# Optimization experiments

Measured on AMD Instinct MI355X. Metric: run time of the kernel, lower is better.

## Reference

```python
import jax, jax.numpy as jnp
import numpy as np
from jax import lax

D_MODEL = 512
NUM_HEADS = 8
HEADDIM = D_MODEL // NUM_HEADS      # 64
EXPAND = 2
D_INNER = EXPAND * D_MODEL          # 1024
D_STATE = 64
NGROUPS = 1
KCONV = 4                           # window_size -> depthwise conv kernel
NHEADS = D_INNER // HEADDIM         # 16 SSM heads
D_FF = 2048
CONV_DIM = D_INNER + 2 * NGROUPS * D_STATE          # 1152 (x, B, C)
D_IN_PROJ = 2 * D_INNER + 2 * NGROUPS * D_STATE + NHEADS  # 2192 (z, x, B, C, dt)
EPS = 1e-6


def _rmsnorm(x, eps=EPS):
    return x * lax.rsqrt(jnp.mean(x * x, axis=-1, keepdims=True) + eps)


def _silu(x):
    return x * jax.nn.sigmoid(x)


def _ssm_scan(xs, dt, A, Bm, Cm):
    # xs: [B,L,H,P], dt: [B,L,H], A: [H], Bm/Cm: [B,L,N]  (ngroups=1 broadcast over heads)
    dA = jnp.exp(dt * A)                 # [B,L,H] decay per step
    dBx = dt[..., None] * xs             # [B,L,H,P] input contribution
    h0 = jnp.zeros((xs.shape[0], xs.shape[2], xs.shape[3], Bm.shape[2]), xs.dtype)

    def step(h, t):
        dA_t, dBx_t, B_t, C_t = t        # [B,H],[B,H,P],[B,N],[B,N]
        h = dA_t[..., None, None] * h + dBx_t[..., None] * B_t[:, None, None, :]
        y = jnp.einsum('bhpn,bn->bhp', h, C_t)
        return h, y

    _, ys = lax.scan(step, h0, (dA.transpose(1, 0, 2), dBx.transpose(1, 0, 2, 3),
                                Bm.transpose(1, 0, 2), Cm.transpose(1, 0, 2)))
    return ys.transpose(1, 0, 2, 3)      # [B,L,H,P]


def setup_inputs() -> dict:
    key = jax.random.key(0)
    ks = jax.random.split(key, 12)
    B, L = 8, 2048
    s = 0.02
    inp = {
        'x': jax.random.normal(ks[0], (B, L, D_MODEL), jnp.float32),
        'mask': jnp.ones((B, L), jnp.float32),
        'W_in': jax.random.normal(ks[1], (D_MODEL, D_IN_PROJ), jnp.float32) * s,
        'conv_w': jax.random.normal(ks[2], (CONV_DIM, KCONV), jnp.float32) * 0.1,
        'conv_b': jnp.zeros((CONV_DIM,), jnp.float32),
        'dt_bias': jax.random.normal(ks[3], (NHEADS,), jnp.float32) * 0.1,
        'A_log': jnp.log(jnp.arange(1, NHEADS + 1, dtype=jnp.float32)),
        'D': jnp.ones((NHEADS,), jnp.float32),
        'norm_w': jnp.ones((D_INNER,), jnp.float32),
        'W_out': jax.random.normal(ks[4], (D_INNER, D_MODEL), jnp.float32) * s,
        'W1': jax.random.normal(ks[5], (D_MODEL, D_FF), jnp.float32) * s,
        'b1': jnp.zeros((D_FF,), jnp.float32),
        'W2': jax.random.normal(ks[6], (D_FF, D_MODEL), jnp.float32) * s,
        'b2': jnp.zeros((D_MODEL,), jnp.float32),
    }
    return inp


def reference(x, mask, W_in, conv_w, conv_b, dt_bias, A_log, D, norm_w, W_out, W1, b1, W2, b2):
    B, L, _ = x.shape
    x = x * mask[..., None]
    u = _rmsnorm(x)

    zxbcdt = u @ W_in                                   # [B,L,2192]
    z = zxbcdt[..., :D_INNER]
    xBC = zxbcdt[..., D_INNER:D_INNER + CONV_DIM]
    dt = zxbcdt[..., D_INNER + CONV_DIM:]               # [B,L,H]

    # causal depthwise conv1d, kernel KCONV
    pad = jnp.pad(xBC, ((0, 0), (KCONV - 1, 0), (0, 0)))
    xBC = sum(pad[:, i:i + L, :] * conv_w[:, i] for i in range(KCONV)) + conv_b
    xBC = _silu(xBC) * mask[..., None]

    xs = xBC[..., :D_INNER].reshape(B, L, NHEADS, HEADDIM)
    Bm = xBC[..., D_INNER:D_INNER + D_STATE]            # [B,L,N] (ngroups=1)
    Cm = xBC[..., D_INNER + D_STATE:]

    dt = jax.nn.softplus(dt + dt_bias)
    A = -jnp.exp(A_log)                                 # [H]

    # bidirectional (non-causal) selective scan: forward + reversed scans
    y_f = _ssm_scan(xs, dt, A, Bm, Cm)
    y_b = _ssm_scan(xs[:, ::-1], dt[:, ::-1], A, Bm[:, ::-1], Cm[:, ::-1])[:, ::-1]
    y = y_f + y_b + D[None, None, :, None] * xs         # [B,L,H,P]
    y = y.reshape(B, L, D_INNER)

    # gated RMSNorm then output projection
    y = _rmsnorm(y * _silu(z)) * norm_w
    m = y @ W_out                                       # mamba2 output, [B,L,D]

    x = m + m                                           # x = x + dropout1(x) with x := mamba out
    h = _rmsnorm(x)
    x = x + (jax.nn.gelu(h @ W1 + b1) @ W2 + b2)        # x + mlp(norm2(x))
    return (x, m, dt, z)
```

## Files before the change

### kernel.cpp

```cpp
#include <hip/hip_runtime.h>
#include <cstdint>
#include <cstddef>

#define L_SEQ   2048
#define NROWS   16384
#define D_MODEL 512
#define D_INNER 1024
#define D_STATE 64
#define NHEADS  16
#define CONV_DIM 1152
#define D_IN_PROJ 2192
#define D_FF 2048
#define EPS 1e-6f

typedef __bf16 bf16_t;
typedef __bf16 bf16x8 __attribute__((ext_vector_type(8)));
typedef __bf16 bf16x4 __attribute__((ext_vector_type(4)));
typedef float  f32x4  __attribute__((ext_vector_type(4)));

#define OFF_WT_IN    0ull
#define OFF_WT_OUT   2244608ull
#define OFF_W1T      3293184ull
#define OFF_W2T      5390336ull
#define OFF_U        7487488ull
#define OFF_XBC_RAW  24264704ull
#define OFF_XBC_CONV 99762176ull
#define OFF_Y2       175259648ull
#define OFF_YN       242368512ull

__device__ __forceinline__ void gl_lds16(const void* g, void* s) {
  __builtin_amdgcn_global_load_lds(
      (__attribute__((address_space(1))) void*)(void*)g,
      (__attribute__((address_space(3))) void*)s, 16, 0, 0);
}

__device__ __forceinline__ float block_sum256(float v, float* red) {
#pragma unroll
  for (int o = 32; o > 0; o >>= 1) v += __shfl_xor(v, o, 64);
  int w = threadIdx.x >> 6;
  if ((threadIdx.x & 63) == 0) red[w] = v;
  __syncthreads();
  return red[0] + red[1] + red[2] + red[3];
}

__device__ __forceinline__ float softplus_f(float x) {
  return (x > 20.f) ? x : log1pf(expf(x));
}
__device__ __forceinline__ float silu_f(float x) {
  return x / (1.f + expf(-x));
}
__device__ __forceinline__ float gelu_tanh_f(float x) {
  float x3 = x * x * x;
  return 0.5f * x * (1.f + tanhf(0.7978845608f * (x + 0.044715f * x3)));
}

__global__ __launch_bounds__(256) void prep_weights_kernel(
    const float* __restrict__ W_in, const float* __restrict__ W_out,
    const float* __restrict__ W1, const float* __restrict__ W2,
    bf16_t* __restrict__ wt_in, bf16_t* __restrict__ wt_out,
    bf16_t* __restrict__ w1t, bf16_t* __restrict__ w2t) {
  const int S1 = D_IN_PROJ * 512;
  const int S2 = 512 * 1024;
  const int S3 = 2048 * 512;
  const int S4 = 512 * 2048;
  const int total = S1 + S2 + S3 + S4;
  for (int i = blockIdx.x * 256 + threadIdx.x; i < total; i += gridDim.x * 256) {
    if (i < S1) {
      int n = i / 512, k = i - n * 512;
      wt_in[i] = (bf16_t)W_in[k * D_IN_PROJ + n];
    } else if (i < S1 + S2) {
      int j = i - S1; int n = j >> 10, k = j & 1023;
      wt_out[j] = (bf16_t)W_out[k * 512 + n];
    } else if (i < S1 + S2 + S3) {
      int j = i - S1 - S2; int n = j >> 9, k = j & 511;
      w1t[j] = (bf16_t)W1[k * 2048 + n];
    } else {
      int j = i - S1 - S2 - S3; int n = j >> 11, k = j & 2047;
      w2t[j] = (bf16_t)W2[k * 512 + n];
    }
  }
}

__global__ __launch_bounds__(256) void rmsnorm_in_kernel(
    const float* __restrict__ x, const float* __restrict__ mask,
    bf16_t* __restrict__ u) {
  __shared__ float red[4];
  int row = blockIdx.x;
  float mk = mask[row];
  const float* xr = x + (size_t)row * 512;
  float v0 = xr[threadIdx.x] * mk;
  float v1 = xr[threadIdx.x + 256] * mk;
  float ss = block_sum256(v0 * v0 + v1 * v1, red);
  float r = rsqrtf(ss * (1.f / 512.f) + EPS);
  bf16_t* ur = u + (size_t)row * 512;
  ur[threadIdx.x] = (bf16_t)(v0 * r);
  ur[threadIdx.x + 256] = (bf16_t)(v1 * r);
}

__global__ __launch_bounds__(256) void rmsnorm2_kernel(
    const float* __restrict__ m, bf16_t* __restrict__ h) {
  __shared__ float red[4];
  int row = blockIdx.x;
  const float* mr = m + (size_t)row * 512;
  float v0 = 2.f * mr[threadIdx.x];
  float v1 = 2.f * mr[threadIdx.x + 256];
  float ss = block_sum256(v0 * v0 + v1 * v1, red);
  float r = rsqrtf(ss * (1.f / 512.f) + EPS);
  bf16_t* hr = h + (size_t)row * 512;
  hr[threadIdx.x] = (bf16_t)(v0 * r);
  hr[threadIdx.x + 256] = (bf16_t)(v1 * r);
}

template <int EPI>
__global__ __launch_bounds__(256, 2) void gemm_kernel(
    const bf16_t* __restrict__ A, const bf16_t* __restrict__ Bt,
    int M, int N, int K,
    float* __restrict__ o0, float* __restrict__ o1, float* __restrict__ o2,
    bf16_t* __restrict__ ob, const float* __restrict__ bias,
    const float* __restrict__ extra) {
  __shared__ bf16_t As[128 * 32];
  __shared__ bf16_t Bs[128 * 32];
  const int tid = threadIdx.x;
  const int lane = tid & 63;
  const int w = tid >> 6;
  const int tileM = blockIdx.y * 128;
  const int tileN = blockIdx.x * 128;

  f32x4 acc[4][4] = {};

  const int wm = (w >> 1) * 64;
  const int wn = (w & 1) * 64;
  const int fr = lane & 15;
  const int fk = (lane >> 4) * 8;

  for (int k0 = 0; k0 < K; k0 += 32) {
    __syncthreads();
#pragma unroll
    for (int i = 0; i < 2; ++i) {
      int rloc = w * 32 + i * 16 + (lane >> 2);
      int cb = (lane & 3) * 16;
      const char* ga = (const char*)(A + (size_t)(tileM + rloc) * K + k0) + cb;
      gl_lds16(ga, (void*)&As[(w * 32 + i * 16) * 32]);
      int rn = tileN + rloc;
      if (rn >= N) rn = N - 1;
      const char* gb = (const char*)(Bt + (size_t)rn * K + k0) + cb;
      gl_lds16(gb, (void*)&Bs[(w * 32 + i * 16) * 32]);
    }
    __syncthreads();

    bf16x8 av[4], bv[4];
#pragma unroll
    for (int i = 0; i < 4; ++i)
      av[i] = *(const bf16x8*)&As[(wm + i * 16 + fr) * 32 + fk];
#pragma unroll
    for (int j = 0; j < 4; ++j)
      bv[j] = *(const bf16x8*)&Bs[(wn + j * 16 + fr) * 32 + fk];
#pragma unroll
    for (int i = 0; i < 4; ++i)
#pragma unroll
      for (int j = 0; j < 4; ++j)
        acc[i][j] = __builtin_amdgcn_mfma_f32_16x16x32_bf16(av[i], bv[j], acc[i][j], 0, 0, 0);
  }

  const int cn = lane & 15;
  const int r0 = (lane >> 4) * 4;
#pragma unroll
  for (int i = 0; i < 4; ++i) {
#pragma unroll
    for (int j = 0; j < 4; ++j) {
      int gn = tileN + wn + j * 16 + cn;
      if (gn >= N) continue;
#pragma unroll
      for (int r = 0; r < 4; ++r) {
        int gm = tileM + wm + i * 16 + r0 + r;
        float v = acc[i][j][r];
        if (EPI == 0) {
          o0[(size_t)gm * N + gn] = v;
        } else if (EPI == 1) {
          if (gn < D_INNER) {
            o0[(size_t)gm * D_INNER + gn] = v;
          } else if (gn < D_INNER + CONV_DIM) {
            o1[(size_t)gm * CONV_DIM + (gn - D_INNER)] = v;
          } else {
            int hh = gn - (D_INNER + CONV_DIM);
            o2[(size_t)gm * NHEADS + hh] = softplus_f(v + bias[hh]);
          }
        } else if (EPI == 2) {
          ob[(size_t)gm * N + gn] = (bf16_t)gelu_tanh_f(v + bias[gn]);
        } else if (EPI == 3) {
          o0[(size_t)gm * N + gn] = v + bias[gn] + 2.f * extra[(size_t)gm * N + gn];
        }
      }
    }
  }
}

__global__ __launch_bounds__(384) void conv_silu_kernel(
    const float* __restrict__ xbc_raw, const float* __restrict__ conv_w,
    const float* __restrict__ conv_b, const float* __restrict__ mask,
    float* __restrict__ xbc_conv) {
  int row = blockIdx.x;
  int t = row & (L_SEQ - 1);
  float mk = mask[row];
#pragma unroll
  for (int k = 0; k < 3; ++k) {
    int c = threadIdx.x + k * 384;
    float4 wv = ((const float4*)conv_w)[c];
    float acc = conv_b[c];
    if (t >= 3) acc += wv.x * xbc_raw[(size_t)(row - 3) * CONV_DIM + c];
    if (t >= 2) acc += wv.y * xbc_raw[(size_t)(row - 2) * CONV_DIM + c];
    if (t >= 1) acc += wv.z * xbc_raw[(size_t)(row - 1) * CONV_DIM + c];
    acc += wv.w * xbc_raw[(size_t)row * CONV_DIM + c];
    xbc_conv[(size_t)row * CONV_DIM + c] = silu_f(acc) * mk;
  }
}


__global__ __launch_bounds__(256) void scan_chunk_kernel(
    const float* __restrict__ xbc, const float* __restrict__ dt_all,
    const float* __restrict__ A_log,
    bf16_t* __restrict__ y2, bf16_t* __restrict__ Tc_buf,
    float* __restrict__ la_buf) {
  const int bid = blockIdx.x;
  const int c = bid & 31, h = (bid >> 5) & 15, b = (bid >> 9) & 7, dir = bid >> 12;
  const float A_h = -expf(A_log[h]);
  const int tid = threadIdx.x, w = tid >> 6, lane = tid & 63;
  const int fr = lane & 15, fk = (lane >> 4) * 8;

  __shared__ __align__(16) bf16_t sB[64][72];
  __shared__ __align__(16) bf16_t sC[64][72];
  __shared__ __align__(16) bf16_t sXt[64][72];
  __shared__ __align__(16) bf16_t sBwt[64][72];
  __shared__ float sLa[64], sDt[64], sW[64];

  const size_t base = (size_t)b * L_SEQ;
#define ROWOF(i) (base + (size_t)(dir ? (L_SEQ - 1 - (c * 64 + (i))) : (c * 64 + (i))))

  if (tid < 64) sDt[tid] = dt_all[ROWOF(tid) * NHEADS + h];

  float bB[16];
#pragma unroll
  for (int r = 0; r < 16; ++r) {
    int i = w * 16 + r;
    const float* src = xbc + ROWOF(i) * CONV_DIM;
    float xv = src[h * 64 + lane];
    float bv = src[D_INNER + lane];
    float cv = src[D_INNER + D_STATE + lane];
    bB[r] = bv;
    sB[i][lane] = (bf16_t)bv;
    sC[i][lane] = (bf16_t)cv;
    sXt[lane][i] = (bf16_t)xv;
  }
  __syncthreads();

  if (w == 0) {
    float v = sDt[lane] * A_h;
#pragma unroll
    for (int d = 1; d < 64; d <<= 1) {
      float o = __shfl_up(v, d, 64);
      if (lane >= d) v += o;
    }
    sLa[lane] = v;
    float la63 = __shfl(v, 63, 64);
    sW[lane] = __expf(la63 - v) * sDt[lane];
  }
  __syncthreads();

#pragma unroll
  for (int r = 0; r < 16; ++r) {
    int i = w * 16 + r;
    sBwt[lane][i] = (bf16_t)(bB[r] * sW[i]);
  }
  if (tid < 64) la_buf[(size_t)bid * 64 + tid] = sLa[tid];

  f32x4 acc1[4] = {};
#pragma unroll
  for (int k0 = 0; k0 < 64; k0 += 32) {
    bf16x8 bv = *(const bf16x8*)&sC[w * 16 + fr][k0 + fk];
#pragma unroll
    for (int mi = 0; mi < 4; ++mi) {
      if (mi <= w) {
        bf16x8 av = *(const bf16x8*)&sB[mi * 16 + fr][k0 + fk];
        acc1[mi] = __builtin_amdgcn_mfma_f32_16x16x32_bf16(av, bv, acc1[mi], 0, 0, 0);
      }
    }
  }
  __syncthreads();

  {
    bf16_t (*sM)[72] = sB;
    float la_t = sLa[w * 16 + fr];
    int t = w * 16 + fr;
#pragma unroll
    for (int mi = 0; mi < 4; ++mi) {
#pragma unroll
      for (int r = 0; r < 4; ++r) {
        int s = mi * 16 + (lane >> 4) * 4 + r;
        float mv = 0.f;
        if (s <= t) mv = acc1[mi][r] * __expf(la_t - sLa[s]) * sDt[s];
        sM[t][s] = (bf16_t)mv;
      }
    }
  }

  f32x4 acc3[4] = {};
#pragma unroll
  for (int k0 = 0; k0 < 64; k0 += 32) {
    bf16x8 bv = *(const bf16x8*)&sBwt[w * 16 + fr][k0 + fk];
#pragma unroll
    for (int mi = 0; mi < 4; ++mi) {
      bf16x8 av = *(const bf16x8*)&sXt[mi * 16 + fr][k0 + fk];
      acc3[mi] = __builtin_amdgcn_mfma_f32_16x16x32_bf16(av, bv, acc3[mi], 0, 0, 0);
    }
  }
  __syncthreads();

  f32x4 acc2[4] = {};
  {
    bf16_t (*sM)[72] = sB;
#pragma unroll
    for (int k0 = 0; k0 < 64; k0 += 32) {
      bf16x8 bv = *(const bf16x8*)&sXt[w * 16 + fr][k0 + fk];
#pragma unroll
      for (int mi = 0; mi < 4; ++mi) {
        bf16x8 av = *(const bf16x8*)&sM[mi * 16 + fr][k0 + fk];
        acc2[mi] = __builtin_amdgcn_mfma_f32_16x16x32_bf16(av, bv, acc2[mi], 0, 0, 0);
      }
    }
  }

  bf16_t* yout = y2 + (size_t)dir * NROWS * D_INNER;
  bf16_t* tco = Tc_buf + (size_t)bid * 4096;
#pragma unroll
  for (int mi = 0; mi < 4; ++mi) {
#pragma unroll
    for (int r = 0; r < 4; ++r) {
      int rowl = mi * 16 + (lane >> 4) * 4 + r;
      int coll = w * 16 + fr;
      yout[ROWOF(rowl) * D_INNER + h * 64 + coll] = (bf16_t)acc2[mi][r];
      tco[rowl * 64 + coll] = (bf16_t)acc3[mi][r];
    }
  }
#undef ROWOF
}

__global__ __launch_bounds__(256) void state_prefix_kernel(
    const float* __restrict__ la_buf, bf16_t* __restrict__ Tc_buf) {
  const int g = blockIdx.x >> 1;
  const int e0 = (blockIdx.x & 1) * 2048 + threadIdx.x * 8;
  bf16_t* tc = Tc_buf + (size_t)g * 32 * 4096 + e0;
  const float* la63 = la_buf + (size_t)g * 32 * 64 + 63;
  float S[8] = {};
  for (int cc = 0; cc < 32; ++cc) {
    bf16x8 t = *(const bf16x8*)(tc + (size_t)cc * 4096);
    float d = __expf(la63[cc * 64]);
    bf16_t sb[8];
#pragma unroll
    for (int j = 0; j < 8; ++j) sb[j] = (bf16_t)S[j];
    *(bf16x8*)(tc + (size_t)cc * 4096) = *(bf16x8*)sb;
    const bf16_t* tp = (const bf16_t*)&t;
#pragma unroll
    for (int j = 0; j < 8; ++j) S[j] = d * S[j] + (float)tp[j];
  }
}

__global__ __launch_bounds__(256) void ystate_kernel(
    const float* __restrict__ xbc, const bf16_t* __restrict__ S_buf,
    const float* __restrict__ la_buf, bf16_t* __restrict__ y2) {
  const int bid = blockIdx.x;
  const int hg = bid & 3, c = (bid >> 2) & 31, b = (bid >> 7) & 7, dir = bid >> 10;
  const int tid = threadIdx.x, w = tid >> 6, lane = tid & 63;
  const int fr = lane & 15, fk = (lane >> 4) * 8;
  const size_t base = (size_t)b * L_SEQ;

  __shared__ __align__(16) bf16_t sC[64][72];
  __shared__ __align__(16) float  sYf[64][72];
  __shared__ float sEla[64];

#pragma unroll
  for (int uu = 0; uu < 4; ++uu) {
    int u = tid + uu * 256;
    int row = u >> 4, q = u & 15;
    int t = c * 64 + row;
    int tr = dir ? (L_SEQ - 1 - t) : t;
    float4 cv = *(const float4*)(xbc + (base + tr) * CONV_DIM + D_INNER + D_STATE + q * 4);
    bf16x4 cb;
    cb[0] = (bf16_t)cv.x; cb[1] = (bf16_t)cv.y; cb[2] = (bf16_t)cv.z; cb[3] = (bf16_t)cv.w;
    *(bf16x4*)&sC[row][q * 4] = cb;
  }
  __syncthreads();

  bf16_t* yout = y2 + (size_t)dir * NROWS * D_INNER;

#pragma unroll 1
  for (int hi = 0; hi < 4; ++hi) {
    const int h = hg * 4 + hi;
    const int bidh = dir * 4096 + b * 512 + h * 32 + c;
    if (tid < 64) sEla[tid] = __expf(la_buf[(size_t)bidh * 64 + tid]);

    const bf16_t* Sp = S_buf + (size_t)bidh * 4096;
    f32x4 acc[4] = {};
#pragma unroll
    for (int k0 = 0; k0 < 64; k0 += 32) {
      bf16x8 bv = *(const bf16x8*)(Sp + (w * 16 + fr) * 64 + k0 + fk);
#pragma unroll
      for (int mi = 0; mi < 4; ++mi) {
        bf16x8 av = *(const bf16x8*)&sC[mi * 16 + fr][k0 + fk];
        acc[mi] = __builtin_amdgcn_mfma_f32_16x16x32_bf16(av, bv, acc[mi], 0, 0, 0);
      }
    }
    __syncthreads();

#pragma unroll
    for (int mi = 0; mi < 4; ++mi) {
#pragma unroll
      for (int r = 0; r < 4; ++r) {
        int tl = mi * 16 + (lane >> 4) * 4 + r;
        sYf[tl][w * 16 + fr] = acc[mi][r] * sEla[tl];
      }
    }
    __syncthreads();

#pragma unroll
    for (int uu = 0; uu < 2; ++uu) {
      int u = tid + uu * 256;
      int row = u >> 3, oct = u & 7;
      int t = c * 64 + row;
      int tr = dir ? (L_SEQ - 1 - t) : t;
      bf16_t* gp = yout + (base + tr) * D_INNER + h * 64 + oct * 8;
      bf16x8 old = *(const bf16x8*)gp;
      const float* yp = &sYf[row][oct * 8];
      bf16x8 nw;
#pragma unroll
      for (int j = 0; j < 8; ++j) nw[j] = (bf16_t)((float)old[j] + yp[j]);
      *(bf16x8*)gp = nw;
    }
  }
}

__global__ __launch_bounds__(256) void combine_kernel(
    const bf16_t* __restrict__ y2, const float* __restrict__ xbc_conv,
    const float* __restrict__ z, const float* __restrict__ Dp,
    const float* __restrict__ norm_w, bf16_t* __restrict__ yn) {
  __shared__ float red[4];
  int row = blockIdx.x;
  const bf16_t* yf = y2 + (size_t)row * D_INNER;
  const bf16_t* yb = y2 + (size_t)NROWS * D_INNER + (size_t)row * D_INNER;
  const float* xs = xbc_conv + (size_t)row * CONV_DIM;
  const float* zr = z + (size_t)row * D_INNER;

  float g[4];
  float ss = 0.f;
#pragma unroll
  for (int k = 0; k < 4; ++k) {
    int c = threadIdx.x + k * 256;
    float v = (float)yf[c] + (float)yb[c] + Dp[c >> 6] * xs[c];
    float gg = v * silu_f(zr[c]);
    g[k] = gg;
    ss += gg * gg;
  }
  ss = block_sum256(ss, red);
  float r = rsqrtf(ss * (1.f / 1024.f) + EPS);
  bf16_t* yr = yn + (size_t)row * D_INNER;
#pragma unroll
  for (int k = 0; k < 4; ++k) {
    int c = threadIdx.x + k * 256;
    yr[c] = (bf16_t)(g[k] * r * norm_w[c]);
  }
}

extern "C" void kernel_launch(void* const* d_in, const int* in_sizes, int n_in,
                              void* d_out, int out_size, void* d_ws, size_t ws_size,
                              hipStream_t stream) {
  const float* x       = (const float*)d_in[0];
  const float* mask    = (const float*)d_in[1];
  const float* W_in    = (const float*)d_in[2];
  const float* conv_w  = (const float*)d_in[3];
  const float* conv_b  = (const float*)d_in[4];
  const float* dt_bias = (const float*)d_in[5];
  const float* A_log   = (const float*)d_in[6];
  const float* Dp      = (const float*)d_in[7];
  const float* norm_w  = (const float*)d_in[8];
  const float* W_out   = (const float*)d_in[9];
  const float* W1      = (const float*)d_in[10];
  const float* b1      = (const float*)d_in[11];
  const float* W2      = (const float*)d_in[12];
  const float* b2      = (const float*)d_in[13];

  float* out_x  = (float*)d_out;
  float* out_m  = out_x + (size_t)NROWS * 512;
  float* out_dt = out_m + (size_t)NROWS * 512;
  float* out_z  = out_dt + (size_t)NROWS * NHEADS;

  char* ws = (char*)d_ws;
  bf16_t* wt_in    = (bf16_t*)(ws + OFF_WT_IN);
  bf16_t* wt_out   = (bf16_t*)(ws + OFF_WT_OUT);
  bf16_t* w1t      = (bf16_t*)(ws + OFF_W1T);
  bf16_t* w2t      = (bf16_t*)(ws + OFF_W2T);
  bf16_t* u_bf     = (bf16_t*)(ws + OFF_U);
  float*  xbc_raw  = (float*)(ws + OFF_XBC_RAW);
  float*  xbc_conv = (float*)(ws + OFF_XBC_CONV);
  bf16_t* y2       = (bf16_t*)(ws + OFF_Y2);
  bf16_t* yn       = (bf16_t*)(ws + OFF_YN);
  bf16_t* h_bf     = u_bf;
  bf16_t* gelu_bf  = (bf16_t*)(ws + OFF_XBC_RAW);
  bf16_t* Tc_buf   = (bf16_t*)(ws + OFF_XBC_RAW);
  float*  la_buf   = (float*)(ws + OFF_U);

  prep_weights_kernel<<<14624, 256, 0, stream>>>(W_in, W_out, W1, W2, wt_in, wt_out, w1t, w2t);
  rmsnorm_in_kernel<<<NROWS, 256, 0, stream>>>(x, mask, u_bf);
  gemm_kernel<1><<<dim3(18, 128), 256, 0, stream>>>(u_bf, wt_in, NROWS, D_IN_PROJ, 512,
                                                    out_z, xbc_raw, out_dt, nullptr, dt_bias, nullptr);
  conv_silu_kernel<<<NROWS, 384, 0, stream>>>(xbc_raw, conv_w, conv_b, mask, xbc_conv);
  scan_chunk_kernel<<<8192, 256, 0, stream>>>(xbc_conv, out_dt, A_log, y2, Tc_buf, la_buf);
  state_prefix_kernel<<<512, 256, 0, stream>>>(la_buf, Tc_buf);
  ystate_kernel<<<2048, 256, 0, stream>>>(xbc_conv, Tc_buf, la_buf, y2);
  combine_kernel<<<NROWS, 256, 0, stream>>>(y2, xbc_conv, out_z, Dp, norm_w, yn);
  gemm_kernel<0><<<dim3(4, 128), 256, 0, stream>>>(yn, wt_out, NROWS, 512, 1024,
                                                   out_m, nullptr, nullptr, nullptr, nullptr, nullptr);
  rmsnorm2_kernel<<<NROWS, 256, 0, stream>>>(out_m, h_bf);
  gemm_kernel<2><<<dim3(16, 128), 256, 0, stream>>>(h_bf, w1t, NROWS, D_FF, 512,
                                                    nullptr, nullptr, nullptr, gelu_bf, b1, nullptr);
  gemm_kernel<3><<<dim3(4, 128), 256, 0, stream>>>(gelu_bf, w2t, NROWS, 512, D_FF,
                                                   out_x, nullptr, nullptr, nullptr, b2, out_m);
}
```

Measured before the change: 677.3 us.

## Double-buffer GEMM LDS tiles with swizzle and stage epilogue through LDS

Restructures the bf16 MFMA GEMM so the next K-tile's global-to-LDS loads are issued into a second buffer while the current tile is computed, with explicit vmcnt waits and barriers. LDS addresses are XOR-swizzled to cut bank conflicts on the fragment reads. The epilogue now stages accumulators through LDS in two halves so each thread writes coalesced 16-byte vectors, with the bias, gelu and softplus epilogues vectorised. The shared memory union is larger, which may reduce occupancy, and the EPI==1 branch selection now assumes each tile falls entirely inside one output segment.

```diff
diff --git a/kernel.cpp b/kernel.cpp
--- a/kernel.cpp
+++ b/kernel.cpp
@@ -118,8 +118,10 @@
     float* __restrict__ o0, float* __restrict__ o1, float* __restrict__ o2,
     bf16_t* __restrict__ ob, const float* __restrict__ bias,
     const float* __restrict__ extra) {
-  __shared__ bf16_t As[128 * 32];
-  __shared__ bf16_t Bs[128 * 32];
+  __shared__ __align__(16) union SMem {
+    struct { bf16_t A[2][128 * 32]; bf16_t B[2][128 * 32]; } t;
+    float ep[64][132];
+  } sm;
   const int tid = threadIdx.x;
   const int lane = tid & 63;
   const int w = tid >> 6;
@@ -132,64 +134,112 @@
   const int wn = (w & 1) * 64;
   const int fr = lane & 15;
   const int fk = (lane >> 4) * 8;
-
-  for (int k0 = 0; k0 < K; k0 += 32) {
-    __syncthreads();
+  const int fks = (fk * 2) ^ (((fr >> 2) & 1) << 4) ^ (((fr >> 3) & 1) << 5);
+
+  const int rsub = lane >> 2;
+  const int cb   = (lane & 3) * 16;
+  const int cbs  = cb ^ (((rsub >> 2) & 1) << 4) ^ (((rsub >> 3) & 1) << 5);
+
+  auto stage = [&](int buf, int k0) {
 #pragma unroll
     for (int i = 0; i < 2; ++i) {
-      int rloc = w * 32 + i * 16 + (lane >> 2);
-      int cb = (lane & 3) * 16;
-      const char* ga = (const char*)(A + (size_t)(tileM + rloc) * K + k0) + cb;
-      gl_lds16(ga, (void*)&As[(w * 32 + i * 16) * 32]);
+      int rloc = w * 32 + i * 16 + rsub;
+      const char* ga = (const char*)(A + (size_t)(tileM + rloc) * K + k0) + cbs;
+      gl_lds16(ga, (void*)&sm.t.A[buf][(w * 32 + i * 16) * 32]);
       int rn = tileN + rloc;
       if (rn >= N) rn = N - 1;
-      const char* gb = (const char*)(Bt + (size_t)rn * K + k0) + cb;
-      gl_lds16(gb, (void*)&Bs[(w * 32 + i * 16) * 32]);
-    }
-    __syncthreads();
+      const char* gb = (const char*)(Bt + (size_t)rn * K + k0) + cbs;
+      gl_lds16(gb, (void*)&sm.t.B[buf][(w * 32 + i * 16) * 32]);
+    }
+  };
+
+  const int nt = K >> 5;
+  stage(0, 0);
+  int cur = 0;
+  for (int t = 0; t < nt; ++t) {
+    if (t + 1 < nt) {
+      stage(cur ^ 1, (t + 1) << 5);
+      asm volatile("s_waitcnt vmcnt(4)" ::: "memory");
+    } else {
+      asm volatile("s_waitcnt vmcnt(0)" ::: "memory");
+    }
+    __builtin_amdgcn_sched_barrier(0);
+    __builtin_amdgcn_s_barrier();
+    __builtin_amdgcn_sched_barrier(0);
 
     bf16x8 av[4], bv[4];
 #pragma unroll
     for (int i = 0; i < 4; ++i)
-      av[i] = *(const bf16x8*)&As[(wm + i * 16 + fr) * 32 + fk];
+      av[i] = *(const bf16x8*)((const char*)&sm.t.A[cur][(wm + i * 16 + fr) * 32] + fks);
 #pragma unroll
     for (int j = 0; j < 4; ++j)
-      bv[j] = *(const bf16x8*)&Bs[(wn + j * 16 + fr) * 32 + fk];
+      bv[j] = *(const bf16x8*)((const char*)&sm.t.B[cur][(wn + j * 16 + fr) * 32] + fks);
 #pragma unroll
     for (int i = 0; i < 4; ++i)
 #pragma unroll
       for (int j = 0; j < 4; ++j)
         acc[i][j] = __builtin_amdgcn_mfma_f32_16x16x32_bf16(av[i], bv[j], acc[i][j], 0, 0, 0);
+
+    __builtin_amdgcn_sched_barrier(0);
+    __builtin_amdgcn_s_barrier();
+    __builtin_amdgcn_sched_barrier(0);
+    cur ^= 1;
   }
 
   const int cn = lane & 15;
   const int r0 = (lane >> 4) * 4;
-#pragma unroll
-  for (int i = 0; i < 4; ++i) {
-#pragma unroll
-    for (int j = 0; j < 4; ++j) {
-      int gn = tileN + wn + j * 16 + cn;
-      if (gn >= N) continue;
-#pragma unroll
-      for (int r = 0; r < 4; ++r) {
-        int gm = tileM + wm + i * 16 + r0 + r;
-        float v = acc[i][j][r];
-        if (EPI == 0) {
-          o0[(size_t)gm * N + gn] = v;
-        } else if (EPI == 1) {
-          if (gn < D_INNER) {
-            o0[(size_t)gm * D_INNER + gn] = v;
-          } else if (gn < D_INNER + CONV_DIM) {
-            o1[(size_t)gm * CONV_DIM + (gn - D_INNER)] = v;
-          } else {
-            int hh = gn - (D_INNER + CONV_DIM);
-            o2[(size_t)gm * NHEADS + hh] = softplus_f(v + bias[hh]);
+  const int myhalf = wm >> 6;
+  const int ef = tid & 31;
+  const int ers = tid >> 5;
+
+#pragma unroll 1
+  for (int ph = 0; ph < 2; ++ph) {
+    __syncthreads();
+    if (myhalf == ph) {
+#pragma unroll
+      for (int i = 0; i < 4; ++i)
+#pragma unroll
+        for (int j = 0; j < 4; ++j)
+#pragma unroll
+          for (int r = 0; r < 4; ++r)
+            sm.ep[i * 16 + r0 + r][wn + j * 16 + cn] = acc[i][j][r];
+    }
+    __syncthreads();
+#pragma unroll
+    for (int pass = 0; pass < 8; ++pass) {
+      int rl = pass * 8 + ers;
+      int gm = tileM + ph * 64 + rl;
+      f32x4 v = *(const f32x4*)&sm.ep[rl][ef * 4];
+      int gn0 = tileN + ef * 4;
+      if (EPI == 0) {
+        *(f32x4*)&o0[(size_t)gm * N + gn0] = v;
+      } else if (EPI == 1) {
+        if (tileN < D_INNER) {
+          *(f32x4*)&o0[(size_t)gm * D_INNER + gn0] = v;
+        } else if (tileN < D_INNER + CONV_DIM) {
+          *(f32x4*)&o1[(size_t)gm * CONV_DIM + (gn0 - D_INNER)] = v;
+        } else {
+          if (ef < 4) {
+            f32x4 d;
+#pragma unroll
+            for (int jj = 0; jj < 4; ++jj)
+              d[jj] = softplus_f(v[jj] + bias[ef * 4 + jj]);
+            *(f32x4*)&o2[(size_t)gm * NHEADS + ef * 4] = d;
           }
-        } else if (EPI == 2) {
-          ob[(size_t)gm * N + gn] = (bf16_t)gelu_tanh_f(v + bias[gn]);
-        } else if (EPI == 3) {
-          o0[(size_t)gm * N + gn] = v + bias[gn] + 2.f * extra[(size_t)gm * N + gn];
         }
+      } else if (EPI == 2) {
+        f32x4 bb = *(const f32x4*)&bias[gn0];
+        bf16x4 o;
+#pragma unroll
+        for (int jj = 0; jj < 4; ++jj) o[jj] = (bf16_t)gelu_tanh_f(v[jj] + bb[jj]);
+        *(bf16x4*)&ob[(size_t)gm * N + gn0] = o;
+      } else {
+        f32x4 bb = *(const f32x4*)&bias[gn0];
+        f32x4 ee = *(const f32x4*)&extra[(size_t)gm * N + gn0];
+        f32x4 o;
+#pragma unroll
+        for (int jj = 0; jj < 4; ++jj) o[jj] = v[jj] + bb[jj] + 2.f * ee[jj];
+        *(f32x4*)&o0[(size_t)gm * N + gn0] = o;
       }
     }
   }
```

New measurement: 676.4 us. Within noise of the previous version (-0.1%).
